# Optimization experiments

Hardware: AMD Instinct MI355X
Metric: run time of the kernel (lower is better)

## Reference

```python
import jax, jax.numpy as jnp
import numpy as np

N_NODES = 100_000
N_RAND_EDGES = 1_600_000
NEG_SLOPE = 0.2


def setup_inputs() -> dict:
    key = jax.random.key(0)
    ks = jax.random.split(key, 12)
    inputs = jax.random.normal(ks[0], (N_NODES, 128), dtype=jnp.float32)
    # params (fc weight [in, H*D], attn vectors [H, D]); 0.1 scale for stability
    W0 = jax.random.normal(ks[1], (128, 4 * 32), dtype=jnp.float32) * 0.1
    al0 = jax.random.normal(ks[2], (4, 32), dtype=jnp.float32) * 0.1
    ar0 = jax.random.normal(ks[3], (4, 32), dtype=jnp.float32) * 0.1
    W1 = jax.random.normal(ks[4], (4 * 32, 4 * 32), dtype=jnp.float32) * 0.1
    al1 = jax.random.normal(ks[5], (4, 32), dtype=jnp.float32) * 0.1
    ar1 = jax.random.normal(ks[6], (4, 32), dtype=jnp.float32) * 0.1
    W2 = jax.random.normal(ks[7], (4 * 32, 1 * 40), dtype=jnp.float32) * 0.1
    al2 = jax.random.normal(ks[8], (1, 40), dtype=jnp.float32) * 0.1
    ar2 = jax.random.normal(ks[9], (1, 40), dtype=jnp.float32) * 0.1
    # edge list: random edges + self loops (guarantees in-degree >= 1)
    src = jnp.concatenate([
        jax.random.randint(ks[10], (N_RAND_EDGES,), 0, N_NODES, dtype=jnp.int32),
        jnp.arange(N_NODES, dtype=jnp.int32)])
    dst = jnp.concatenate([
        jax.random.randint(ks[11], (N_RAND_EDGES,), 0, N_NODES, dtype=jnp.int32),
        jnp.arange(N_NODES, dtype=jnp.int32)])
    return dict(inputs=inputs, W0=W0, al0=al0, ar0=ar0, W1=W1, al1=al1,
                ar1=ar1, W2=W2, al2=al2, ar2=ar2, src=src, dst=dst, empty=0)


def _gat_conv(h, W, al, ar, src, dst):
    """DGL-style GATConv (no dropout, no residual, no bias). Returns [N, H, D]."""
    N = h.shape[0]
    H, D = al.shape
    feat = (h @ W).reshape(N, H, D)
    el = jnp.sum(feat * al, axis=-1)  # [N, H]
    er = jnp.sum(feat * ar, axis=-1)  # [N, H]
    e = jax.nn.leaky_relu(el[src] + er[dst], negative_slope=NEG_SLOPE)  # [E, H]
    # edge softmax over incoming edges of each destination node (stable)
    m = jax.ops.segment_max(e, dst, num_segments=N)          # [N, H]
    ee = jnp.exp(e - m[dst])                                 # [E, H]
    denom = jax.ops.segment_sum(ee, dst, num_segments=N)     # [N, H]
    alpha = ee / denom[dst]                                  # [E, H]
    # gather source features, weight by attention, scatter-sum to destinations
    out = jax.ops.segment_sum(feat[src] * alpha[:, :, None], dst, num_segments=N)
    return out


def reference(inputs, W0, al0, ar0, W1, al1, ar1, W2, al2, ar2, src, dst, empty):
    N = inputs.shape[0]
    h = inputs
    for (W, al, ar) in ((W0, al0, ar0), (W1, al1, ar1)):
        h = jax.nn.elu(_gat_conv(h, W, al, ar, src, dst)).reshape(N, -1)
    logits = _gat_conv(h, W2, al2, ar2, src, dst).mean(axis=1)  # [N, num_classes]
    return jax.nn.log_softmax(logits, axis=1)
```

## Files before the change

kernel.cpp:

```cpp
#include <hip/hip_runtime.h>
#include <math.h>

typedef unsigned int uint32;

__device__ inline uint32 bf16rn(float x){
  uint32 b = __float_as_uint(x);
  return (b + 0x7fffu + ((b>>16)&1u)) >> 16;
}
__device__ inline float bf16lo(uint32 v){ return __uint_as_float(v<<16); }
__device__ inline float bf16hi(uint32 v){ return __uint_as_float(v & 0xffff0000u); }

#define BKT_SHIFT 9
#define BKTCAP 12288
#define PCHUNK 8192

__global__ __launch_bounds__(256) void k_partition(const int* __restrict__ src, const int* __restrict__ dst,
                        int* __restrict__ bkt_cursor, uint32* __restrict__ pairs, int E){
  __shared__ int cnt[512];
  __shared__ int base[512];
  int t = threadIdx.x;
  int blockBase = blockIdx.x * PCHUNK;
  for (int i=t; i<512; i+=256) cnt[i]=0;
  __syncthreads();
  #pragma unroll
  for (int i=0; i<PCHUNK/1024; i++){
    int e0 = blockBase + (i*256 + t)*4;
    if (e0+3 < E){
      int4 d4 = *(const int4*)&dst[e0];
      atomicAdd(&cnt[d4.x>>BKT_SHIFT],1);
      atomicAdd(&cnt[d4.y>>BKT_SHIFT],1);
      atomicAdd(&cnt[d4.z>>BKT_SHIFT],1);
      atomicAdd(&cnt[d4.w>>BKT_SHIFT],1);
    } else {
      for (int e=e0; e<E && e<e0+4; e++) atomicAdd(&cnt[dst[e]>>BKT_SHIFT],1);
    }
  }
  __syncthreads();
  for (int i=t; i<512; i+=256){
    int c = cnt[i];
    base[i] = c ? atomicAdd(&bkt_cursor[i], c) : 0;
    cnt[i] = 0;
  }
  __syncthreads();
  #pragma unroll
  for (int i=0; i<PCHUNK/1024; i++){
    int e0 = blockBase + (i*256 + t)*4;
    if (e0+3 < E){
      int4 s4 = *(const int4*)&src[e0];
      int4 d4 = *(const int4*)&dst[e0];
      int bx, pos;
      bx=d4.x>>BKT_SHIFT; pos=base[bx]+atomicAdd(&cnt[bx],1); if(pos<BKTCAP) pairs[(size_t)bx*BKTCAP+pos]=(uint32)s4.x|((uint32)(d4.x&511)<<22);
      bx=d4.y>>BKT_SHIFT; pos=base[bx]+atomicAdd(&cnt[bx],1); if(pos<BKTCAP) pairs[(size_t)bx*BKTCAP+pos]=(uint32)s4.y|((uint32)(d4.y&511)<<22);
      bx=d4.z>>BKT_SHIFT; pos=base[bx]+atomicAdd(&cnt[bx],1); if(pos<BKTCAP) pairs[(size_t)bx*BKTCAP+pos]=(uint32)s4.z|((uint32)(d4.z&511)<<22);
      bx=d4.w>>BKT_SHIFT; pos=base[bx]+atomicAdd(&cnt[bx],1); if(pos<BKTCAP) pairs[(size_t)bx*BKTCAP+pos]=(uint32)s4.w|((uint32)(d4.w&511)<<22);
    } else {
      for (int e=e0; e<E && e<e0+4; e++){
        int s=src[e], d=dst[e];
        int bx=d>>BKT_SHIFT; int pos=base[bx]+atomicAdd(&cnt[bx],1);
        if(pos<BKTCAP) pairs[(size_t)bx*BKTCAP+pos]=(uint32)s|((uint32)(d&511)<<22);
      }
    }
  }
}

__global__ __launch_bounds__(512) void k_scanbkt(const int* __restrict__ bkt_cursor, int nb,
                      int* __restrict__ bucket_base, int* __restrict__ row_ptr, int N){
  __shared__ int sc[512];
  int t = threadIdx.x;
  int v = (t<nb) ? min(bkt_cursor[t], BKTCAP) : 0;
  sc[t]=v; __syncthreads();
  int x=v;
  for (int off=1; off<512; off<<=1){
    int y=(t>=off)? sc[t-off]:0;
    __syncthreads();
    x+=y; sc[t]=x;
    __syncthreads();
  }
  if (t<nb) bucket_base[t] = x - v;
  if (t==511) row_ptr[N] = x;
}

__global__ __launch_bounds__(1024) void k_build(const int* __restrict__ bkt_cursor,
                        const int* __restrict__ bucket_base, const uint32* __restrict__ pairs,
                        int* __restrict__ row_ptr, int* __restrict__ csr_src, int N){
  __shared__ int hist[512];
  __shared__ int sc[512];
  __shared__ int cur[512];
  int b = blockIdx.x;
  int t = threadIdx.x;
  int cnt = bkt_cursor[b]; if (cnt > BKTCAP) cnt = BKTCAP;
  int base = bucket_base[b];
  const uint32* p = pairs + (size_t)b*BKTCAP;
  if (t<512) hist[t]=0;
  __syncthreads();
  for (int i=t; i<cnt; i+=1024) atomicAdd(&hist[p[i]>>22], 1);
  __syncthreads();
  int v = (t<512)? hist[t] : 0;
  if (t<512) sc[t]=v;
  __syncthreads();
  int x=v;
  for (int off=1; off<512; off<<=1){
    int y = (t<512 && t>=off)? sc[t-off] : 0;
    __syncthreads();
    if (t<512){ x+=y; sc[t]=x; }
    __syncthreads();
  }
  if (t<512){
    int excl = x - v;
    int gnode = (b<<BKT_SHIFT) + t;
    if (gnode < N) row_ptr[gnode] = base + excl;
    cur[t] = excl;
  }
  __syncthreads();
  for (int i=t; i<cnt; i+=1024){
    uint32 e = p[i];
    int pos = atomicAdd(&cur[e>>22], 1);
    csr_src[base + pos] = (int)(e & 0x3FFFFFu);
  }
}

__global__ __launch_bounds__(256) void k_gemm128(const float* __restrict__ A, const float* __restrict__ W,
                                                 const float* __restrict__ al, const float* __restrict__ ar,
                                                 unsigned short* __restrict__ Fb,
                                                 float* __restrict__ el, float* __restrict__ er, int N){
  __shared__ float hs[32][68];
  __shared__ float ws[32][128];
  int t = threadIdx.x;
  int rowBase = blockIdx.x*64;
  int rg8 = (t>>5)*8;
  int cq  = (t&31)*4;
  float acc[8][4] = {};
  for (int kc=0; kc<128; kc+=32){
    {
      int row = t>>2; int kk = (t&3)*8;
      int grow = rowBase+row;
      float4 v0, v1;
      if (grow < N){
        v0 = *(const float4*)&A[(size_t)grow*128 + kc + kk];
        v1 = *(const float4*)&A[(size_t)grow*128 + kc + kk + 4];
      } else { v0 = make_float4(0,0,0,0); v1 = v0; }
      hs[kk+0][row]=v0.x; hs[kk+1][row]=v0.y; hs[kk+2][row]=v0.z; hs[kk+3][row]=v0.w;
      hs[kk+4][row]=v1.x; hs[kk+5][row]=v1.y; hs[kk+6][row]=v1.z; hs[kk+7][row]=v1.w;
    }
    {
      int k = t>>3; int c0 = (t&7)*16;
      const float4* wp = (const float4*)&W[(size_t)(kc+k)*128 + c0];
      float4 w0=wp[0], w1=wp[1], w2=wp[2], w3=wp[3];
      *(float4*)&ws[k][c0+ 0]=w0; *(float4*)&ws[k][c0+ 4]=w1;
      *(float4*)&ws[k][c0+ 8]=w2; *(float4*)&ws[k][c0+12]=w3;
    }
    __syncthreads();
    #pragma unroll
    for (int k=0;k<32;k++){
      float4 bv  = *(const float4*)&ws[k][cq];
      float4 av0 = *(const float4*)&hs[k][rg8];
      float4 av1 = *(const float4*)&hs[k][rg8+4];
      float a8[8] = {av0.x,av0.y,av0.z,av0.w,av1.x,av1.y,av1.z,av1.w};
      float b4[4] = {bv.x,bv.y,bv.z,bv.w};
      #pragma unroll
      for (int r=0;r<8;r++)
        #pragma unroll
        for (int c=0;c<4;c++)
          acc[r][c] = fmaf(a8[r], b4[c], acc[r][c]);
    }
    __syncthreads();
  }
  float al4[4], ar4[4];
  #pragma unroll
  for (int i=0;i<4;i++){ al4[i]=al[cq+i]; ar4[i]=ar[cq+i]; }
  int c = t&31;
  int h = c>>3;
  int rowTop = rowBase + rg8;
  #pragma unroll
  for (int r=0;r<8;r++){
    int row = rowTop + r;
    if (row < N){
      uint32 u0 = bf16rn(acc[r][0]) | (bf16rn(acc[r][1])<<16);
      uint32 u1 = bf16rn(acc[r][2]) | (bf16rn(acc[r][3])<<16);
      *(uint2*)(Fb + (size_t)row*128 + cq) = make_uint2(u0,u1);
    }
    float pl = acc[r][0]*al4[0]+acc[r][1]*al4[1]+acc[r][2]*al4[2]+acc[r][3]*al4[3];
    float pr = acc[r][0]*ar4[0]+acc[r][1]*ar4[1]+acc[r][2]*ar4[2]+acc[r][3]*ar4[3];
    pl += __shfl_xor(pl,1); pr += __shfl_xor(pr,1);
    pl += __shfl_xor(pl,2); pr += __shfl_xor(pr,2);
    pl += __shfl_xor(pl,4); pr += __shfl_xor(pr,4);
    if ((c&7)==0 && row < N){ el[(size_t)row*4+h]=pl; er[(size_t)row*4+h]=pr; }
  }
}

#define AGG_STEP(sY) { int s_=(sY); \
    float x_=el[(size_t)s_*4+h]+erv; x_=x_>0.f?x_:0.2f*x_; x_=__expf(x_); \
    uint32 v_=Fu[(size_t)s_*64+lane]; \
    denom+=x_; acc0=fmaf(x_,bf16lo(v_),acc0); acc1=fmaf(x_,bf16hi(v_),acc1); }

__global__ __launch_bounds__(256) void k_agg128(const uint32* __restrict__ Fu, const float* __restrict__ el,
                         const float* __restrict__ er, const int* __restrict__ row_ptr,
                         const int* __restrict__ csr_src, float* __restrict__ out, int N){
  int node = (blockIdx.x*blockDim.x + threadIdx.x)>>6;
  int lane = threadIdx.x & 63;
  if (node >= N) return;
  int h = lane>>4;
  float erv = er[(size_t)node*4+h];
  int beg = row_ptr[node], end = row_ptr[node+1];
  int deg = end - beg;
  int sv = (beg + lane < end) ? csr_src[beg+lane] : 0;
  float acc0=0.f, acc1=0.f, denom=0.f;
  int nmain = deg > 64 ? 64 : deg;
  int i = 0;
  for (; i+8 <= nmain; i+=8){
    int s0=__shfl(sv,i+0), s1=__shfl(sv,i+1), s2=__shfl(sv,i+2), s3=__shfl(sv,i+3);
    int s4=__shfl(sv,i+4), s5=__shfl(sv,i+5), s6=__shfl(sv,i+6), s7=__shfl(sv,i+7);
    AGG_STEP(s0); AGG_STEP(s1); AGG_STEP(s2); AGG_STEP(s3);
    AGG_STEP(s4); AGG_STEP(s5); AGG_STEP(s6); AGG_STEP(s7);
  }
  for (; i<nmain; i++){ int s=__shfl(sv,i); AGG_STEP(s); }
  if (deg > 64){
    for (int e=beg+64; e<end; e++){ int s=csr_src[e]; AGG_STEP(s); }
  }
  float inv = 1.0f/denom;
  float o0 = acc0*inv, o1 = acc1*inv;
  o0 = o0>0.f ? o0 : expm1f(o0);
  o1 = o1>0.f ? o1 : expm1f(o1);
  *(float2*)&out[(size_t)node*128 + lane*2] = make_float2(o0,o1);
}

__global__ __launch_bounds__(256) void k_gemm42(const float* __restrict__ A, const float* __restrict__ W,
                        const float* __restrict__ al, const float* __restrict__ ar,
                        unsigned short* __restrict__ Fb, float* __restrict__ el, float* __restrict__ er, int N){
  __shared__ float wfull[128*48];
  __shared__ float hs[32][132];
  int t = threadIdx.x;
  int rowBase = blockIdx.x*128;
  for (int i=t; i<1280; i+=256){
    float4 v = *(const float4*)&W[i*4];
    int g = i*4;
    *(float4*)&wfull[(g/40)*48 + (g%40)] = v;
  }
  {
    int k = t & 127;
    const float* wrow = W + k*40;
    const float* a = (t < 128) ? al : ar;
    float s = 0.f;
    #pragma unroll
    for (int c=0;c<40;c++) s += wrow[c]*a[c];
    if (t < 128){
      wfull[k*48+40] = s;
      wfull[k*48+42] = 0.f; wfull[k*48+43] = 0.f; wfull[k*48+44] = 0.f;
    } else {
      wfull[k*48+41] = s;
      wfull[k*48+45] = 0.f; wfull[k*48+46] = 0.f; wfull[k*48+47] = 0.f;
    }
  }
  int c0 = (t&7)*6;
  int r0 = (t>>3)*4;
  float acc[4][6] = {};
  for (int kc=0; kc<128; kc+=32){
    {
      int row = t>>1; int kk0 = (t&1)*16;
      int grow = rowBase + row;
      #pragma unroll
      for (int j=0;j<4;j++){
        float4 v = (grow<N) ? *(const float4*)&A[(size_t)grow*128 + kc + kk0 + 4*j] : make_float4(0,0,0,0);
        hs[kk0+4*j+0][row]=v.x; hs[kk0+4*j+1][row]=v.y; hs[kk0+4*j+2][row]=v.z; hs[kk0+4*j+3][row]=v.w;
      }
    }
    __syncthreads();
    #pragma unroll
    for (int k=0;k<32;k++){
      float4 av = *(const float4*)&hs[k][r0];
      const float* wp = &wfull[(kc+k)*48 + c0];
      float2 b01 = *(const float2*)&wp[0];
      float2 b23 = *(const float2*)&wp[2];
      float2 b45 = *(const float2*)&wp[4];
      float a4[4] = {av.x,av.y,av.z,av.w};
      float b6[6] = {b01.x,b01.y,b23.x,b23.y,b45.x,b45.y};
      #pragma unroll
      for (int r=0;r<4;r++)
        #pragma unroll
        for (int c=0;c<6;c++)
          acc[r][c] = fmaf(a4[r], b6[c], acc[r][c]);
    }
    __syncthreads();
  }
  #pragma unroll
  for (int r=0;r<4;r++){
    int row = rowBase + r0 + r;
    if (row >= N) break;
    if (c0 < 40){
      #pragma unroll
      for (int j=0;j<6;j+=2){
        int col = c0 + j;
        if (col < 40){
          uint32 u = bf16rn(acc[r][j]) | (bf16rn(acc[r][j+1])<<16);
          *(uint32*)(Fb + (size_t)row*40 + col) = u;
        }
      }
      if (c0 == 36){ el[row] = acc[r][4]; er[row] = acc[r][5]; }
    }
  }
}

__global__ __launch_bounds__(256) void k_agg40(const unsigned short* __restrict__ Fb, const float* __restrict__ el,
                       const float* __restrict__ er, const int* __restrict__ row_ptr,
                       const int* __restrict__ csr_src, float* __restrict__ out, int N){
  int node = (blockIdx.x*blockDim.x + threadIdx.x)>>6;
  int lane = threadIdx.x & 63;
  if (node >= N) return;
  bool act = lane<40;
  int l40 = act ? lane : 0;
  float erv = er[node];
  int beg = row_ptr[node], end = row_ptr[node+1];
  int deg = end - beg;
  int sv = (beg + lane < end) ? csr_src[beg+lane] : 0;
  float acc=0.f, denom=0.f;
  int nmain = deg > 64 ? 64 : deg;
  int i = 0;
  for (; i+4 <= nmain; i+=4){
    int s0=__shfl(sv,i+0), s1=__shfl(sv,i+1), s2=__shfl(sv,i+2), s3=__shfl(sv,i+3);
    float e0=el[s0], e1=el[s1], e2=el[s2], e3=el[s3];
    unsigned short f0=Fb[(size_t)s0*40+l40], f1=Fb[(size_t)s1*40+l40];
    unsigned short f2=Fb[(size_t)s2*40+l40], f3=Fb[(size_t)s3*40+l40];
    float x;
    x=e0+erv; x=x>0.f?x:0.2f*x; x=__expf(x); denom+=x; acc=fmaf(x,__uint_as_float(((uint32)f0)<<16),acc);
    x=e1+erv; x=x>0.f?x:0.2f*x; x=__expf(x); denom+=x; acc=fmaf(x,__uint_as_float(((uint32)f1)<<16),acc);
    x=e2+erv; x=x>0.f?x:0.2f*x; x=__expf(x); denom+=x; acc=fmaf(x,__uint_as_float(((uint32)f2)<<16),acc);
    x=e3+erv; x=x>0.f?x:0.2f*x; x=__expf(x); denom+=x; acc=fmaf(x,__uint_as_float(((uint32)f3)<<16),acc);
  }
  for (; i<nmain; i++){
    int s=__shfl(sv,i);
    float x=el[s]+erv; x=x>0.f?x:0.2f*x; x=__expf(x);
    unsigned short f=Fb[(size_t)s*40+l40];
    denom+=x; acc=fmaf(x,__uint_as_float(((uint32)f)<<16),acc);
  }
  if (deg > 64){
    for (int e=beg+64; e<end; e++){
      int s=csr_src[e];
      float x=el[s]+erv; x=x>0.f?x:0.2f*x; x=__expf(x);
      unsigned short f=Fb[(size_t)s*40+l40];
      denom+=x; acc=fmaf(x,__uint_as_float(((uint32)f)<<16),acc);
    }
  }
  float logit = acc/denom;
  float m = act ? logit : -INFINITY;
  for (int off=32; off; off>>=1) m = fmaxf(m, __shfl_xor(m, off));
  float ex = act ? expf(logit - m) : 0.f;
  float ssum = ex;
  for (int off=32; off; off>>=1) ssum += __shfl_xor(ssum, off);
  if (act) out[(size_t)node*40 + lane] = logit - m - logf(ssum);
}

extern "C" void kernel_launch(void* const* d_in, const int* in_sizes, int n_in,
                              void* d_out, int out_size, void* d_ws, size_t ws_size,
                              hipStream_t stream){
  const float* inputs = (const float*)d_in[0];
  const float* W0  = (const float*)d_in[1];
  const float* al0 = (const float*)d_in[2];
  const float* ar0 = (const float*)d_in[3];
  const float* W1  = (const float*)d_in[4];
  const float* al1 = (const float*)d_in[5];
  const float* ar1 = (const float*)d_in[6];
  const float* W2  = (const float*)d_in[7];
  const float* al2 = (const float*)d_in[8];
  const float* ar2 = (const float*)d_in[9];
  const int* src = (const int*)d_in[10];
  const int* dst = (const int*)d_in[11];
  int N = in_sizes[0]/128;
  int E = in_sizes[10];
  int NB = (N + (1<<BKT_SHIFT) - 1) >> BKT_SHIFT;

  char* p = (char*)d_ws;
  auto carve = [&](size_t bytes)->char*{ char* q=p; p += ((bytes+255)/256)*256; return q; };
  unsigned short* Fb   = (unsigned short*)carve((size_t)N*128*2);
  unsigned short* Fb40 = (unsigned short*)carve((size_t)N*40*2);
  float* bufH = (float*)carve((size_t)N*128*4);
  float* el  = (float*)carve((size_t)N*4*4);
  float* er  = (float*)carve((size_t)N*4*4);
  float* el2 = (float*)carve((size_t)N*4);
  float* er2 = (float*)carve((size_t)N*4);
  int* bkt_cursor  = (int*)carve((size_t)NB*4);
  int* bucket_base = (int*)carve((size_t)NB*4);
  int* row_ptr = (int*)carve((size_t)(N+1)*4);
  int* csr_src = (int*)carve((size_t)E*4);

  uint32* pairs = (uint32*)bufH;

  hipMemsetAsync(bkt_cursor, 0, (size_t)NB*4, stream);
  int nPB = (E + PCHUNK - 1) / PCHUNK;
  k_partition<<<nPB, 256, 0, stream>>>(src, dst, bkt_cursor, pairs, E);
  k_scanbkt  <<<1, 512, 0, stream>>>(bkt_cursor, NB, bucket_base, row_ptr, N);
  k_build    <<<NB, 1024, 0, stream>>>(bkt_cursor, bucket_base, pairs, row_ptr, csr_src, N);

  int gRows = (N+63)/64;
  int gWave = (N+3)/4;
  int gRows42 = (N+127)/128;
  k_gemm128<<<gRows,256,0,stream>>>(inputs, W0, al0, ar0, Fb, el, er, N);
  k_agg128 <<<gWave,256,0,stream>>>((const uint32*)Fb, el, er, row_ptr, csr_src, bufH, N);
  k_gemm128<<<gRows,256,0,stream>>>(bufH, W1, al1, ar1, Fb, el, er, N);
  k_agg128 <<<gWave,256,0,stream>>>((const uint32*)Fb, el, er, row_ptr, csr_src, bufH, N);
  k_gemm42 <<<gRows42,256,0,stream>>>(bufH, W2, al2, ar2, Fb40, el2, er2, N);
  k_agg40  <<<gWave,256,0,stream>>>(Fb40, el2, er2, row_ptr, csr_src, (float*)d_out, N);
}
```

Before: 412.4 us.

## Precompute edge attention weights cooperatively and stream sources via uniform loads

In both aggregation kernels, each lane now computes the exp attention weight for one edge (grouped per head in the 128-wide kernel) up front. The weights are reduced with shuffles to get the denominator and stored in LDS. The main loop then reads source indices through wave-uniform pointer loads (readfirstlane on the row bounds) and weights from LDS, so the redundant per-lane el gather and exp for every edge is gone. This trades repeated transcendental and scattered el loads for an LDS staging step, and keeps scalar index loads instead of cross-lane shuffles.

Result: no change. 409.2 us (-0.8%).

```diff
diff --git a/kernel.cpp b/kernel.cpp
--- a/kernel.cpp
+++ b/kernel.cpp
@@ -188,36 +188,80 @@
   }
 }
 
-#define AGG_STEP(sY) { int s_=(sY); \
-    float x_=el[(size_t)s_*4+h]+erv; x_=x_>0.f?x_:0.2f*x_; x_=__expf(x_); \
-    uint32 v_=Fu[(size_t)s_*64+lane]; \
-    denom+=x_; acc0=fmaf(x_,bf16lo(v_),acc0); acc1=fmaf(x_,bf16hi(v_),acc1); }
-
 __global__ __launch_bounds__(256) void k_agg128(const uint32* __restrict__ Fu, const float* __restrict__ el,
                          const float* __restrict__ er, const int* __restrict__ row_ptr,
                          const int* __restrict__ csr_src, float* __restrict__ out, int N){
-  int node = (blockIdx.x*blockDim.x + threadIdx.x)>>6;
-  int lane = threadIdx.x & 63;
-  if (node >= N) return;
+  __shared__ float wlds[4][272];
+  int t = threadIdx.x;
+  int lane = t & 63;
+  int wv = t >> 6;
+  int node = (blockIdx.x*blockDim.x + t)>>6;
+  if (__builtin_amdgcn_readfirstlane(node) >= N) return;
   int h = lane>>4;
+  int i0 = lane & 15;
   float erv = er[(size_t)node*4+h];
   int beg = row_ptr[node], end = row_ptr[node+1];
-  int deg = end - beg;
-  int sv = (beg + lane < end) ? csr_src[beg+lane] : 0;
-  float acc0=0.f, acc1=0.f, denom=0.f;
-  int nmain = deg > 64 ? 64 : deg;
-  int i = 0;
-  for (; i+8 <= nmain; i+=8){
-    int s0=__shfl(sv,i+0), s1=__shfl(sv,i+1), s2=__shfl(sv,i+2), s3=__shfl(sv,i+3);
-    int s4=__shfl(sv,i+4), s5=__shfl(sv,i+5), s6=__shfl(sv,i+6), s7=__shfl(sv,i+7);
-    AGG_STEP(s0); AGG_STEP(s1); AGG_STEP(s2); AGG_STEP(s3);
-    AGG_STEP(s4); AGG_STEP(s5); AGG_STEP(s6); AGG_STEP(s7);
-  }
-  for (; i<nmain; i++){ int s=__shfl(sv,i); AGG_STEP(s); }
-  if (deg > 64){
-    for (int e=beg+64; e<end; e++){ int s=csr_src[e]; AGG_STEP(s); }
-  }
-  float inv = 1.0f/denom;
+  int ubeg = __builtin_amdgcn_readfirstlane(beg);
+  int uend = __builtin_amdgcn_readfirstlane(end);
+  int udeg = uend - ubeg;
+  int sv = (lane < udeg) ? csr_src[ubeg+lane] : 0;
+  float w4[4];
+  #pragma unroll
+  for (int j=0;j<4;j++){
+    int eidx = i0 + 16*j;
+    int sn = __shfl(sv, eidx);
+    float x = 0.f;
+    if (eidx < udeg){
+      float ev = el[(size_t)sn*4+h] + erv;
+      ev = ev>0.f ? ev : 0.2f*ev;
+      x = __expf(ev);
+    }
+    w4[j] = x;
+  }
+  float dsum = (w4[0]+w4[1]) + (w4[2]+w4[3]);
+  dsum += __shfl_xor(dsum, 1);
+  dsum += __shfl_xor(dsum, 2);
+  dsum += __shfl_xor(dsum, 4);
+  dsum += __shfl_xor(dsum, 8);
+  int wb = h*68 + i0;
+  wlds[wv][wb   ] = w4[0];
+  wlds[wv][wb+16] = w4[1];
+  wlds[wv][wb+32] = w4[2];
+  wlds[wv][wb+48] = w4[3];
+  const int* sp = csr_src + ubeg;
+  const float* wp = &wlds[wv][h*68];
+  float acc0=0.f, acc1=0.f;
+  int nm = udeg > 64 ? 64 : udeg;
+  int i=0;
+  for (; i+8<=nm; i+=8){
+    #pragma unroll
+    for (int k=0;k<8;k++){
+      int s = sp[i+k];
+      float wi = wp[i+k];
+      uint32 v = Fu[(size_t)s*64 + lane];
+      acc0 = fmaf(wi, bf16lo(v), acc0);
+      acc1 = fmaf(wi, bf16hi(v), acc1);
+    }
+  }
+  for (; i<nm; i++){
+    int s = sp[i];
+    float wi = wp[i];
+    uint32 v = Fu[(size_t)s*64 + lane];
+    acc0 = fmaf(wi, bf16lo(v), acc0);
+    acc1 = fmaf(wi, bf16hi(v), acc1);
+  }
+  if (udeg > 64){
+    for (int e=64; e<udeg; e++){
+      int s = sp[e];
+      float x = el[(size_t)s*4+h] + erv;
+      x = x>0.f?x:0.2f*x; x=__expf(x);
+      uint32 v = Fu[(size_t)s*64+lane];
+      dsum += x;
+      acc0 = fmaf(x, bf16lo(v), acc0);
+      acc1 = fmaf(x, bf16hi(v), acc1);
+    }
+  }
+  float inv = 1.0f/dsum;
   float o0 = acc0*inv, o1 = acc1*inv;
   o0 = o0>0.f ? o0 : expm1f(o0);
   o1 = o1>0.f ? o1 : expm1f(o1);
@@ -303,44 +347,64 @@
 __global__ __launch_bounds__(256) void k_agg40(const unsigned short* __restrict__ Fb, const float* __restrict__ el,
                        const float* __restrict__ er, const int* __restrict__ row_ptr,
                        const int* __restrict__ csr_src, float* __restrict__ out, int N){
-  int node = (blockIdx.x*blockDim.x + threadIdx.x)>>6;
-  int lane = threadIdx.x & 63;
-  if (node >= N) return;
+  __shared__ float wlds[4][64];
+  int t = threadIdx.x;
+  int lane = t & 63;
+  int wv = t >> 6;
+  int node = (blockIdx.x*blockDim.x + t)>>6;
+  if (__builtin_amdgcn_readfirstlane(node) >= N) return;
   bool act = lane<40;
   int l40 = act ? lane : 0;
   float erv = er[node];
   int beg = row_ptr[node], end = row_ptr[node+1];
-  int deg = end - beg;
-  int sv = (beg + lane < end) ? csr_src[beg+lane] : 0;
-  float acc=0.f, denom=0.f;
-  int nmain = deg > 64 ? 64 : deg;
-  int i = 0;
-  for (; i+4 <= nmain; i+=4){
-    int s0=__shfl(sv,i+0), s1=__shfl(sv,i+1), s2=__shfl(sv,i+2), s3=__shfl(sv,i+3);
-    float e0=el[s0], e1=el[s1], e2=el[s2], e3=el[s3];
-    unsigned short f0=Fb[(size_t)s0*40+l40], f1=Fb[(size_t)s1*40+l40];
-    unsigned short f2=Fb[(size_t)s2*40+l40], f3=Fb[(size_t)s3*40+l40];
-    float x;
-    x=e0+erv; x=x>0.f?x:0.2f*x; x=__expf(x); denom+=x; acc=fmaf(x,__uint_as_float(((uint32)f0)<<16),acc);
-    x=e1+erv; x=x>0.f?x:0.2f*x; x=__expf(x); denom+=x; acc=fmaf(x,__uint_as_float(((uint32)f1)<<16),acc);
-    x=e2+erv; x=x>0.f?x:0.2f*x; x=__expf(x); denom+=x; acc=fmaf(x,__uint_as_float(((uint32)f2)<<16),acc);
-    x=e3+erv; x=x>0.f?x:0.2f*x; x=__expf(x); denom+=x; acc=fmaf(x,__uint_as_float(((uint32)f3)<<16),acc);
-  }
-  for (; i<nmain; i++){
-    int s=__shfl(sv,i);
-    float x=el[s]+erv; x=x>0.f?x:0.2f*x; x=__expf(x);
-    unsigned short f=Fb[(size_t)s*40+l40];
-    denom+=x; acc=fmaf(x,__uint_as_float(((uint32)f)<<16),acc);
-  }
-  if (deg > 64){
-    for (int e=beg+64; e<end; e++){
-      int s=csr_src[e];
-      float x=el[s]+erv; x=x>0.f?x:0.2f*x; x=__expf(x);
-      unsigned short f=Fb[(size_t)s*40+l40];
-      denom+=x; acc=fmaf(x,__uint_as_float(((uint32)f)<<16),acc);
-    }
-  }
-  float logit = acc/denom;
+  int ubeg = __builtin_amdgcn_readfirstlane(beg);
+  int uend = __builtin_amdgcn_readfirstlane(end);
+  int udeg = uend - ubeg;
+  int sv = (lane < udeg) ? csr_src[ubeg+lane] : 0;
+  float w = 0.f;
+  if (lane < udeg){
+    float ev = el[sv] + erv;
+    ev = ev>0.f ? ev : 0.2f*ev;
+    w = __expf(ev);
+  }
+  float dsum = w;
+  dsum += __shfl_xor(dsum, 1);
+  dsum += __shfl_xor(dsum, 2);
+  dsum += __shfl_xor(dsum, 4);
+  dsum += __shfl_xor(dsum, 8);
+  dsum += __shfl_xor(dsum, 16);
+  dsum += __shfl_xor(dsum, 32);
+  wlds[wv][lane] = w;
+  const int* sp = csr_src + ubeg;
+  float acc=0.f;
+  int nm = udeg > 64 ? 64 : udeg;
+  int i=0;
+  for (; i+8<=nm; i+=8){
+    #pragma unroll
+    for (int k=0;k<8;k++){
+      int s = sp[i+k];
+      float wi = wlds[wv][i+k];
+      unsigned short f = Fb[(size_t)s*40 + l40];
+      acc = fmaf(wi, __uint_as_float(((uint32)f)<<16), acc);
+    }
+  }
+  for (; i<nm; i++){
+    int s = sp[i];
+    float wi = wlds[wv][i];
+    unsigned short f = Fb[(size_t)s*40 + l40];
+    acc = fmaf(wi, __uint_as_float(((uint32)f)<<16), acc);
+  }
+  if (udeg > 64){
+    for (int e=64; e<udeg; e++){
+      int s = sp[e];
+      float x = el[s] + erv;
+      x = x>0.f?x:0.2f*x; x=__expf(x);
+      unsigned short f = Fb[(size_t)s*40 + l40];
+      dsum += x;
+      acc = fmaf(x, __uint_as_float(((uint32)f)<<16), acc);
+    }
+  }
+  float logit = acc/dsum;
   float m = act ? logit : -INFINITY;
   for (int off=32; off; off>>=1) m = fmaxf(m, __shfl_xor(m, off));
   float ex = act ? expf(logit - m) : 0.f;
```
